# Kernel tuning notes

Measured on AMD Instinct MI355X. Metric: run time of the kernel, lower is better.

Reference implementation:

```python
import jax, jax.numpy as jnp
import numpy as np

N_GLIMPSES = 3
GS = 64          # glimpse_size
IN_C = 3         # input_channels
B, H, W = 64, 512, 512


def get_glimpses(image, loc):
    """Multi-scale glimpse extraction (tf.image.extract_glimpse, centered+normalized)
    followed by antialiased bicubic resize to GS x GS, concatenated on channels."""
    b, h, w, c = image.shape
    max_size = GS * 2 ** (N_GLIMPSES - 1)
    padded = jnp.pad(image, ((0, 0), (max_size, max_size), (max_size, max_size), (0, 0)))
    hp, wp = h + 2 * max_size, w + 2 * max_size
    # normalized+centered offsets: (-1,-1)=upper-left, (1,1)=lower-right of padded image
    center = (loc + 1.0) * 0.5 * jnp.array([hp, wp], dtype=jnp.float32)  # (y, x) per batch
    glimpses = []
    for i in range(N_GLIMPSES):
        s = GS * 2 ** i  # current crop size (python int, static)
        tl = jnp.round(center - 0.5 * s).astype(jnp.int32)
        tl = jnp.clip(tl, 0, jnp.array([hp - s, wp - s], dtype=jnp.int32))

        def slice_one(img, yx):
            return jax.lax.dynamic_slice(img, (yx[0], yx[1], 0), (s, s, c))

        g = jax.vmap(slice_one)(padded, tl)                      # [B, s, s, C]
        g = jax.image.resize(g, (b, GS, GS, c), method='cubic')  # antialiased bicubic
        glimpses.append(g)
    return jnp.concatenate(glimpses, axis=-1)  # [B, GS, GS, N_GLIMPSES*C]


def setup_inputs() -> dict:
    key = jax.random.key(0)
    ks = jax.random.split(key, 10)
    image = jax.random.uniform(ks[0], (B, H, W, IN_C), dtype=jnp.float32)
    loc = jax.random.uniform(ks[1], (B, 2), dtype=jnp.float32, minval=-1.0, maxval=1.0)
    cg = N_GLIMPSES * IN_C
    # conv1_g: full-kernel (GS x GS) valid conv -> 1x1x128
    Wg = jax.random.normal(ks[2], (GS, GS, cg, 128), dtype=jnp.float32) * (1.0 / np.sqrt(GS * GS * cg))
    bg = jnp.zeros((128,), jnp.float32)
    # conv1_l: 1x1 conv on loc [B,1,1,2]
    Wl = jax.random.normal(ks[3], (2, 128), dtype=jnp.float32) * (1.0 / np.sqrt(2.0))
    bl = jnp.zeros((128,), jnp.float32)
    # out: 1x1 conv 128 -> 256
    Wo = jax.random.normal(ks[4], (128, 256), dtype=jnp.float32) * (1.0 / np.sqrt(128.0))
    bo = jnp.zeros((256,), jnp.float32)
    return {"image": image, "loc": loc, "Wg": Wg, "bg": bg, "Wl": Wl, "bl": bl, "Wo": Wo, "bo": bo}


def reference(image, loc, Wg, bg, Wl, bl, Wo, bo):
    glimpses = get_glimpses(image, loc)  # [B, GS, GS, N_GLIMPSES*IN_C]
    # conv1_g with kernel == glimpse size and VALID padding == dense contraction over hwc
    x1 = jax.nn.relu(jnp.einsum('bhwc,hwck->bk', glimpses, Wg) + bg)  # [B,128]
    x2 = jax.nn.relu(loc @ Wl + bl)                                   # [B,128]
    out = jax.nn.relu((x1 + x2) @ Wo + bo)                            # [B,256]
    return out
```

## Files before the change

kernel.cpp:

```cpp
#include <hip/hip_runtime.h>

#define IMG_H 512
#define IMG_W 512
#define PAD   256
#define HP    1024
#define BATCH 64
#define KTOT  36864
#define KTILE 144
#define KB    16
#define NTILES 256

__device__ __forceinline__ float keys_cubic(float x) {
  if (x >= 2.0f) return 0.0f;
  if (x >= 1.0f) return ((-0.5f * x + 2.5f) * x - 4.0f) * x + 2.0f;
  return ((1.5f * x - 2.5f) * x) * x + 1.0f;
}

__device__ __forceinline__ int iclamp(int v, int lo, int hi) {
  return min(max(v, lo), hi);
}

__global__ __launch_bounds__(256) void glimpse_kernel(
    const float* __restrict__ img, const float* __restrict__ loc,
    float* __restrict__ G) {
  __shared__ float tmp1[384];
  __shared__ float tmp2[768];
  const int y   = blockIdx.x & 63;
  const int b   = blockIdx.x >> 6;
  const int tid = threadIdx.x;

  const float cy = (loc[2 * b] + 1.0f) * 0.5f * 1024.0f;
  const float cx = (loc[2 * b + 1] + 1.0f) * 0.5f * 1024.0f;
  const int tly0 = iclamp((int)rintf(cy - 32.0f), 0, HP - 64);
  const int tlx0 = iclamp((int)rintf(cx - 32.0f), 0, HP - 64);
  const int tly1 = iclamp((int)rintf(cy - 64.0f), 0, HP - 128);
  const int tlx1 = iclamp((int)rintf(cx - 64.0f), 0, HP - 128);
  const int tly2 = iclamp((int)rintf(cy - 128.0f), 0, HP - 256);
  const int tlx2 = iclamp((int)rintf(cx - 128.0f), 0, HP - 256);
  const float* imb  = img + (size_t)b * (IMG_H * IMG_W * 3);
  float*       Grow = G + ((size_t)b * 64 + y) * (64 * 9);

  if (tid < 192) {
    int x = tid / 3, c = tid - 3 * (tid / 3);
    int py = tly0 + y - PAD, px = tlx0 + x - PAD;
    float v = 0.0f;
    if ((unsigned)py < (unsigned)IMG_H && (unsigned)px < (unsigned)IMG_W)
      v = imb[(py * IMG_W + px) * 3 + c];
    Grow[x * 9 + c] = v;
  }

  float wy1[8];
  int iy0_1;
  {
    float sy = ((float)y + 0.5f) * 2.0f - 0.5f;
    iy0_1 = (int)ceilf(sy - 4.0f);
    float ws = 0.0f;
#pragma unroll
    for (int t = 0; t < 8; ++t) {
      int i = iy0_1 + t;
      float w = (i >= 0 && i < 128) ? keys_cubic(fabsf(sy - (float)i) * 0.5f) : 0.0f;
      wy1[t] = w;
      ws += w;
    }
    float wi = 1.0f / ws;
#pragma unroll
    for (int t = 0; t < 8; ++t) wy1[t] *= wi;
  }
  float wy2[16];
  int iy0_2;
  {
    float sy = ((float)y + 0.5f) * 4.0f - 0.5f;
    iy0_2 = (int)ceilf(sy - 8.0f);
    float ws = 0.0f;
#pragma unroll
    for (int t = 0; t < 16; ++t) {
      int i = iy0_2 + t;
      float w = (i >= 0 && i < 256) ? keys_cubic(fabsf(sy - (float)i) * 0.25f) : 0.0f;
      wy2[t] = w;
      ws += w;
    }
    float wi = 1.0f / ws;
#pragma unroll
    for (int t = 0; t < 16; ++t) wy2[t] *= wi;
  }

  for (int e = tid; e < 384; e += 256) {
    int x = e / 3, c = e - 3 * (e / 3);
    int px = tlx1 - PAD + x;
    float a = 0.0f;
    if ((unsigned)px < (unsigned)IMG_W) {
      const float* colp = imb + (px * 3 + c);
#pragma unroll
      for (int t = 0; t < 8; ++t) {
        int py = tly1 + iy0_1 + t - PAD;
        if ((unsigned)py < (unsigned)IMG_H)
          a = fmaf(wy1[t], colp[py * (IMG_W * 3)], a);
      }
    }
    tmp1[e] = a;
  }
  for (int e = tid; e < 768; e += 256) {
    int x = e / 3, c = e - 3 * (e / 3);
    int px = tlx2 - PAD + x;
    float a = 0.0f;
    if ((unsigned)px < (unsigned)IMG_W) {
      const float* colp = imb + (px * 3 + c);
#pragma unroll
      for (int t = 0; t < 16; ++t) {
        int py = tly2 + iy0_2 + t - PAD;
        if ((unsigned)py < (unsigned)IMG_H)
          a = fmaf(wy2[t], colp[py * (IMG_W * 3)], a);
      }
    }
    tmp2[e] = a;
  }
  __syncthreads();

  for (int o = tid; o < 384; o += 256) {
    int oo = (o >= 192) ? o - 192 : o;
    int xo = oo / 3, c = oo - 3 * xo;
    if (o < 192) {
      float sx  = ((float)xo + 0.5f) * 2.0f - 0.5f;
      int   ix0 = (int)ceilf(sx - 4.0f);
      float a = 0.0f, wsx = 0.0f;
#pragma unroll
      for (int t = 0; t < 8; ++t) {
        int i = ix0 + t;
        if (i >= 0 && i < 128) {
          float w = keys_cubic(fabsf(sx - (float)i) * 0.5f);
          wsx += w;
          a = fmaf(w, tmp1[i * 3 + c], a);
        }
      }
      Grow[xo * 9 + 3 + c] = a / wsx;
    } else {
      float sx  = ((float)xo + 0.5f) * 4.0f - 0.5f;
      int   ix0 = (int)ceilf(sx - 8.0f);
      float a = 0.0f, wsx = 0.0f;
#pragma unroll
      for (int t = 0; t < 16; ++t) {
        int i = ix0 + t;
        if (i >= 0 && i < 256) {
          float w = keys_cubic(fabsf(sx - (float)i) * 0.25f);
          wsx += w;
          a = fmaf(w, tmp2[i * 3 + c], a);
        }
      }
      Grow[xo * 9 + 6 + c] = a / wsx;
    }
  }
}

__global__ __launch_bounds__(256) void gemm_kernel(
    const float* __restrict__ G, const float* __restrict__ Wg,
    float* __restrict__ partials) {
  const int tile = blockIdx.x;
  const int tid  = threadIdx.x;
  const int tn   = tid & 15;
  const int tm   = tid >> 4;
  __shared__ float Gs[2][KB][64];
  __shared__ float Ws[2][KB][128];

  const int gb = tid >> 2;
  const int gj = (tid & 3) * 4;
  const int wr = tid >> 4;
  const int wc = (tid & 15) * 8;
  const size_t gbase = (size_t)gb * KTOT + (size_t)tile * KTILE + gj;
  const size_t wbase = ((size_t)tile * KTILE + wr) * 128 + wc;

  float4 g4 = *(const float4*)(G + gbase);
  float4 wa = *(const float4*)(Wg + wbase);
  float4 wb = *(const float4*)(Wg + wbase + 4);

  float acc[4][8];
#pragma unroll
  for (int mi = 0; mi < 4; ++mi)
#pragma unroll
    for (int ni = 0; ni < 8; ++ni) acc[mi][ni] = 0.0f;

  constexpr int NCHUNK = KTILE / KB;
#pragma unroll
  for (int chunk = 0; chunk < NCHUNK; ++chunk) {
    const int buf = chunk & 1;
    Gs[buf][gj + 0][gb] = g4.x;
    Gs[buf][gj + 1][gb] = g4.y;
    Gs[buf][gj + 2][gb] = g4.z;
    Gs[buf][gj + 3][gb] = g4.w;
    *(float4*)&Ws[buf][wr][wc]     = wa;
    *(float4*)&Ws[buf][wr][wc + 4] = wb;
    __syncthreads();
    if (chunk + 1 < NCHUNK) {
      g4 = *(const float4*)(G + gbase + (chunk + 1) * KB);
      wa = *(const float4*)(Wg + wbase + (size_t)(chunk + 1) * KB * 128);
      wb = *(const float4*)(Wg + wbase + (size_t)(chunk + 1) * KB * 128 + 4);
    }
#pragma unroll
    for (int j = 0; j < KB; ++j) {
      float4 gv = *(const float4*)&Gs[buf][j][tm * 4];
      float4 w0 = *(const float4*)&Ws[buf][j][tn * 8];
      float4 w1 = *(const float4*)&Ws[buf][j][tn * 8 + 4];
      float gm[4] = {gv.x, gv.y, gv.z, gv.w};
      float wn[8] = {w0.x, w0.y, w0.z, w0.w, w1.x, w1.y, w1.z, w1.w};
#pragma unroll
      for (int mi = 0; mi < 4; ++mi)
#pragma unroll
        for (int ni = 0; ni < 8; ++ni)
          acc[mi][ni] = fmaf(gm[mi], wn[ni], acc[mi][ni]);
    }
  }

#pragma unroll
  for (int mi = 0; mi < 4; ++mi) {
    int m = tm * 4 + mi;
    float* dst = partials + ((size_t)m * NTILES + tile) * 128 + tn * 8;
    *(float4*)dst       = make_float4(acc[mi][0], acc[mi][1], acc[mi][2], acc[mi][3]);
    *(float4*)(dst + 4) = make_float4(acc[mi][4], acc[mi][5], acc[mi][6], acc[mi][7]);
  }
}

__global__ __launch_bounds__(256) void finalize_kernel(
    const float* __restrict__ partials, const float* __restrict__ loc,
    const float* __restrict__ bg, const float* __restrict__ Wl,
    const float* __restrict__ bl, const float* __restrict__ Wo,
    const float* __restrict__ bo, float* __restrict__ out) {
  const int b   = blockIdx.x;
  const int tid = threadIdx.x;

  const float4* base = (const float4*)(partials + (size_t)b * NTILES * 128);
  float4 acc = make_float4(0.f, 0.f, 0.f, 0.f);
#pragma unroll 8
  for (int i = 0; i < 32; ++i) {
    float4 v = base[(size_t)i * 256 + tid];
    acc.x += v.x; acc.y += v.y; acc.z += v.z; acc.w += v.w;
  }

  __shared__ float red[8][128];
  __shared__ float h[128];
  {
    float* r = &red[tid >> 5][(tid & 31) * 4];
    r[0] = acc.x; r[1] = acc.y; r[2] = acc.z; r[3] = acc.w;
  }
  __syncthreads();
  if (tid < 128) {
    float ss = 0.0f;
#pragma unroll
    for (int g = 0; g < 8; ++g) ss += red[g][tid];
    float x1 = fmaxf(ss + bg[tid], 0.0f);
    float x2 = fmaxf(fmaf(loc[2 * b], Wl[tid],
                          fmaf(loc[2 * b + 1], Wl[128 + tid], bl[tid])),
                     0.0f);
    h[tid] = x1 + x2;
  }
  __syncthreads();
  {
    int n = tid;
    float a = bo[n];
#pragma unroll 8
    for (int kk = 0; kk < 128; ++kk) a = fmaf(h[kk], Wo[kk * 256 + n], a);
    out[(size_t)b * 256 + n] = fmaxf(a, 0.0f);
  }
}

extern "C" void kernel_launch(void* const* d_in, const int* in_sizes, int n_in,
                              void* d_out, int out_size, void* d_ws, size_t ws_size,
                              hipStream_t stream) {
  const float* img = (const float*)d_in[0];
  const float* loc = (const float*)d_in[1];
  const float* Wg  = (const float*)d_in[2];
  const float* bg  = (const float*)d_in[3];
  const float* Wl  = (const float*)d_in[4];
  const float* bl  = (const float*)d_in[5];
  const float* Wo  = (const float*)d_in[6];
  const float* bo  = (const float*)d_in[7];
  float* out = (float*)d_out;

  float* ws = (float*)d_ws;
  float* G        = ws;
  float* partials = ws + 2359296;

  glimpse_kernel<<<BATCH * 64, 256, 0, stream>>>(img, loc, G);
  gemm_kernel<<<NTILES, 256, 0, stream>>>(G, Wg, partials);
  finalize_kernel<<<BATCH, 256, 0, stream>>>(partials, loc, bg, Wl, bl, Wo, bo, out);
}
```

Measured before the change: 318.8 us.

## Store glimpses as bf16 and use MFMA bf16 for the glimpse GEMM

```diff
diff --git a/kernel.cpp b/kernel.cpp
--- a/kernel.cpp
+++ b/kernel.cpp
@@ -1,4 +1,5 @@
 #include <hip/hip_runtime.h>
+#include <hip/hip_bf16.h>
 
 #define IMG_H 512
 #define IMG_W 512
@@ -6,9 +7,12 @@
 #define HP    1024
 #define BATCH 64
 #define KTOT  36864
-#define KTILE 144
-#define KB    16
-#define NTILES 256
+#define KTILE 96
+#define NTILES 384
+#define GSTRIDE 104
+
+typedef __attribute__((ext_vector_type(8))) short short8;
+typedef __attribute__((ext_vector_type(4))) float f32x4;
 
 __device__ __forceinline__ float keys_cubic(float x) {
   if (x >= 2.0f) return 0.0f;
@@ -19,10 +23,16 @@
 __device__ __forceinline__ int iclamp(int v, int lo, int hi) {
   return min(max(v, lo), hi);
 }
+__device__ __forceinline__ unsigned short f2bits(float f) {
+  __hip_bfloat16 h = __float2bfloat16(f);
+  unsigned short s;
+  __builtin_memcpy(&s, &h, 2);
+  return s;
+}
 
 __global__ __launch_bounds__(256) void glimpse_kernel(
     const float* __restrict__ img, const float* __restrict__ loc,
-    float* __restrict__ G) {
+    unsigned short* __restrict__ G) {
   __shared__ float tmp1[384];
   __shared__ float tmp2[768];
   const int y   = blockIdx.x & 63;
@@ -37,8 +47,8 @@
   const int tlx1 = iclamp((int)rintf(cx - 64.0f), 0, HP - 128);
   const int tly2 = iclamp((int)rintf(cy - 128.0f), 0, HP - 256);
   const int tlx2 = iclamp((int)rintf(cx - 128.0f), 0, HP - 256);
-  const float* imb  = img + (size_t)b * (IMG_H * IMG_W * 3);
-  float*       Grow = G + ((size_t)b * 64 + y) * (64 * 9);
+  const float* imb = img + (size_t)b * (IMG_H * IMG_W * 3);
+  unsigned short* Grow = G + ((size_t)b * 64 + y) * (64 * 9);
 
   if (tid < 192) {
     int x = tid / 3, c = tid - 3 * (tid / 3);
@@ -46,7 +56,7 @@
     float v = 0.0f;
     if ((unsigned)py < (unsigned)IMG_H && (unsigned)px < (unsigned)IMG_W)
       v = imb[(py * IMG_W + px) * 3 + c];
-    Grow[x * 9 + c] = v;
+    Grow[x * 9 + c] = f2bits(v);
   }
 
   float wy1[8];
@@ -132,7 +142,7 @@
           a = fmaf(w, tmp1[i * 3 + c], a);
         }
       }
-      Grow[xo * 9 + 3 + c] = a / wsx;
+      Grow[xo * 9 + 3 + c] = f2bits(a / wsx);
     } else {
       float sx  = ((float)xo + 0.5f) * 4.0f - 0.5f;
       int   ix0 = (int)ceilf(sx - 8.0f);
@@ -146,76 +156,79 @@
           a = fmaf(w, tmp2[i * 3 + c], a);
         }
       }
-      Grow[xo * 9 + 6 + c] = a / wsx;
+      Grow[xo * 9 + 6 + c] = f2bits(a / wsx);
     }
   }
 }
 
 __global__ __launch_bounds__(256) void gemm_kernel(
-    const float* __restrict__ G, const float* __restrict__ Wg,
+    const unsigned short* __restrict__ G, const float* __restrict__ Wg,
     float* __restrict__ partials) {
+  __shared__ __align__(16) unsigned short Gs[64 * GSTRIDE];
+  const int tid  = threadIdx.x;
   const int tile = blockIdx.x;
-  const int tid  = threadIdx.x;
-  const int tn   = tid & 15;
-  const int tm   = tid >> 4;
-  __shared__ float Gs[2][KB][64];
-  __shared__ float Ws[2][KB][128];
-
-  const int gb = tid >> 2;
-  const int gj = (tid & 3) * 4;
-  const int wr = tid >> 4;
-  const int wc = (tid & 15) * 8;
-  const size_t gbase = (size_t)gb * KTOT + (size_t)tile * KTILE + gj;
-  const size_t wbase = ((size_t)tile * KTILE + wr) * 128 + wc;
-
-  float4 g4 = *(const float4*)(G + gbase);
-  float4 wa = *(const float4*)(Wg + wbase);
-  float4 wb = *(const float4*)(Wg + wbase + 4);
-
-  float acc[4][8];
-#pragma unroll
-  for (int mi = 0; mi < 4; ++mi)
-#pragma unroll
-    for (int ni = 0; ni < 8; ++ni) acc[mi][ni] = 0.0f;
-
-  constexpr int NCHUNK = KTILE / KB;
-#pragma unroll
-  for (int chunk = 0; chunk < NCHUNK; ++chunk) {
-    const int buf = chunk & 1;
-    Gs[buf][gj + 0][gb] = g4.x;
-    Gs[buf][gj + 1][gb] = g4.y;
-    Gs[buf][gj + 2][gb] = g4.z;
-    Gs[buf][gj + 3][gb] = g4.w;
-    *(float4*)&Ws[buf][wr][wc]     = wa;
-    *(float4*)&Ws[buf][wr][wc + 4] = wb;
-    __syncthreads();
-    if (chunk + 1 < NCHUNK) {
-      g4 = *(const float4*)(G + gbase + (chunk + 1) * KB);
-      wa = *(const float4*)(Wg + wbase + (size_t)(chunk + 1) * KB * 128);
-      wb = *(const float4*)(Wg + wbase + (size_t)(chunk + 1) * KB * 128 + 4);
-    }
-#pragma unroll
-    for (int j = 0; j < KB; ++j) {
-      float4 gv = *(const float4*)&Gs[buf][j][tm * 4];
-      float4 w0 = *(const float4*)&Ws[buf][j][tn * 8];
-      float4 w1 = *(const float4*)&Ws[buf][j][tn * 8 + 4];
-      float gm[4] = {gv.x, gv.y, gv.z, gv.w};
-      float wn[8] = {w0.x, w0.y, w0.z, w0.w, w1.x, w1.y, w1.z, w1.w};
-#pragma unroll
-      for (int mi = 0; mi < 4; ++mi)
-#pragma unroll
-        for (int ni = 0; ni < 8; ++ni)
-          acc[mi][ni] = fmaf(gm[mi], wn[ni], acc[mi][ni]);
-    }
-  }
-
-#pragma unroll
-  for (int mi = 0; mi < 4; ++mi) {
-    int m = tm * 4 + mi;
-    float* dst = partials + ((size_t)m * NTILES + tile) * 128 + tn * 8;
-    *(float4*)dst       = make_float4(acc[mi][0], acc[mi][1], acc[mi][2], acc[mi][3]);
-    *(float4*)(dst + 4) = make_float4(acc[mi][4], acc[mi][5], acc[mi][6], acc[mi][7]);
-  }
+  const int kt   = tile * KTILE;
+
+  {
+    const int m = tid >> 2, i = tid & 3;
+    const unsigned short* src = G + (size_t)m * KTOT + kt;
+    unsigned short* dst = Gs + m * GSTRIDE;
+#pragma unroll
+    for (int p = 0; p < 3; ++p) {
+      const int o8 = (i + 4 * p) * 8;
+      *(float4*)(dst + o8) = *(const float4*)(src + o8);
+    }
+  }
+  __syncthreads();
+
+  const int lane = tid & 63;
+  const int wv   = tid >> 6;
+  const int ln   = lane & 15;
+  const int q    = lane >> 4;
+  const int nb   = wv * 32 + ln;
+
+  f32x4 acc[4][2];
+#pragma unroll
+  for (int mt = 0; mt < 4; ++mt)
+#pragma unroll
+    for (int nt = 0; nt < 2; ++nt) {
+      acc[mt][nt][0] = 0.f; acc[mt][nt][1] = 0.f;
+      acc[mt][nt][2] = 0.f; acc[mt][nt][3] = 0.f;
+    }
+
+#pragma unroll
+  for (int s = 0; s < KTILE / 32; ++s) {
+    short8 af[4];
+#pragma unroll
+    for (int mt = 0; mt < 4; ++mt)
+      af[mt] = *(const short8*)(Gs + (mt * 16 + ln) * GSTRIDE + s * 32 + q * 8);
+    short8 bf[2];
+#pragma unroll
+    for (int nt = 0; nt < 2; ++nt) {
+      const float* wp = Wg + (size_t)(kt + s * 32 + q * 8) * 128 + nb + nt * 16;
+      short8 v;
+#pragma unroll
+      for (int j = 0; j < 8; ++j) v[j] = (short)f2bits(wp[j * 128]);
+      bf[nt] = v;
+    }
+#pragma unroll
+    for (int mt = 0; mt < 4; ++mt)
+#pragma unroll
+      for (int nt = 0; nt < 2; ++nt)
+        acc[mt][nt] = __builtin_amdgcn_mfma_f32_16x16x32_bf16(
+            af[mt], bf[nt], acc[mt][nt], 0, 0, 0);
+  }
+
+#pragma unroll
+  for (int mt = 0; mt < 4; ++mt)
+#pragma unroll
+    for (int nt = 0; nt < 2; ++nt)
+#pragma unroll
+      for (int i = 0; i < 4; ++i) {
+        const int row = mt * 16 + q * 4 + i;
+        const int col = nb + nt * 16;
+        partials[((size_t)row * NTILES + tile) * 128 + col] = acc[mt][nt][i];
+      }
 }
 
 __global__ __launch_bounds__(256) void finalize_kernel(
@@ -229,7 +242,7 @@
   const float4* base = (const float4*)(partials + (size_t)b * NTILES * 128);
   float4 acc = make_float4(0.f, 0.f, 0.f, 0.f);
 #pragma unroll 8
-  for (int i = 0; i < 32; ++i) {
+  for (int i = 0; i < 48; ++i) {
     float4 v = base[(size_t)i * 256 + tid];
     acc.x += v.x; acc.y += v.y; acc.z += v.z; acc.w += v.w;
   }
@@ -253,7 +266,7 @@
   }
   __syncthreads();
   {
-    int n = tid;
+    const int n = tid;
     float a = bo[n];
 #pragma unroll 8
     for (int kk = 0; kk < 128; ++kk) a = fmaf(h[kk], Wo[kk * 256 + n], a);
@@ -274,9 +287,9 @@
   const float* bo  = (const float*)d_in[7];
   float* out = (float*)d_out;
 
-  float* ws = (float*)d_ws;
-  float* G        = ws;
-  float* partials = ws + 2359296;
+  char* ws = (char*)d_ws;
+  unsigned short* G = (unsigned short*)ws;
+  float* partials   = (float*)(ws + 2359296 * 2);
 
   glimpse_kernel<<<BATCH * 64, 256, 0, stream>>>(img, loc, G);
   gemm_kernel<<<NTILES, 256, 0, stream>>>(G, Wg, partials);
```

After: 315.1 us. About the same (-1.2%).
